# Optimization experiments

Hardware: AMD Instinct MI355X
Metric: run time of the kernel (lower is better)

## Reference

```python
import jax, jax.numpy as jnp
import numpy as np

NB_RADIUSES = 24
SIGMA = 0.1


def setup_inputs() -> dict:
    key = jax.random.key(0)
    k1, k2, k3 = jax.random.split(key, 3)
    nb, nf, nx, ny, nz = 2, 2, 256, 256, 16
    x = jax.random.uniform(k1, (nb, nf, nx, ny, nz), dtype=jnp.float32)
    # center of mass: real part is the column coordinate (in [0, ny)),
    # imag part is the row coordinate (in [0, nx)) -- keep centers inside the plane
    com_real = jax.random.uniform(k2, (nb, nf, nz), dtype=jnp.float32) * ny
    com_imag = jax.random.uniform(k3, (nb, nf, nz), dtype=jnp.float32) * nx
    return {"x": x, "com_real": com_real, "com_imag": com_imag}


def reference(x, com_real, com_imag):
    nb, nf, nx, ny, nz = x.shape
    # complex plan: real = index % ny (column), imag = index // ny (row)
    col = jnp.arange(ny, dtype=jnp.float32)   # real axis
    row = jnp.arange(nx, dtype=jnp.float32)   # imag axis
    # centered plan, broadcast to (nb, nf, nx, ny, nz)
    dx = col[None, None, None, :, None] - com_real[:, :, None, None, :]
    dy = row[None, None, :, None, None] - com_imag[:, :, None, None, :]
    theta = jnp.arctan2(dy, dx)           # arg(centered_plan)
    theta_neg = jnp.arctan2(-dy, -dx)     # arg(-centered_plan)

    # angles i*(2pi/nr) - pi; branch selection identical to the torch code
    angles = np.arange(NB_RADIUSES) * (2.0 * np.pi / NB_RADIUSES) - np.pi
    use_neg = (angles > 0.5 * np.pi) | (angles < -0.5 * np.pi)
    targets = np.where(angles > 0.5 * np.pi, angles - np.pi,
                       np.where(angles < -0.5 * np.pi, angles + np.pi, angles))
    use_neg = jnp.asarray(use_neg)
    targets = jnp.asarray(targets.astype(np.float32))

    # select angle field per radius: (R, nb, nf, nx, ny, nz)
    sel = jnp.where(use_neg[:, None, None, None, None, None],
                    theta_neg[None], theta[None])
    coef = jnp.float32(1.0 / (SIGMA * np.sqrt(2.0 * np.pi)))
    diff = sel - targets[:, None, None, None, None, None]
    w = coef * jnp.exp(-(diff ** 2) / jnp.float32(2.0 * SIGMA ** 2))

    # gaussian-weighted reduction over the (x, y) plane, keep z
    s = jnp.einsum('Rbfxyz,bfxyz->bfRz', w, x)
    return jnp.sqrt(2.0 * s)
```

## Files before the change

kernel.cpp:

```cpp
#include <hip/hip_runtime.h>
#include <math.h>

#define NR 24
#define NBATCH 2
#define NFEAT 2
#define NX 256
#define NY 256
#define NZ 16

constexpr double DPI = 3.141592653589793;

struct Tgts { float t[NR]; int neg[NR]; };

constexpr Tgts make_tgts() {
    Tgts r{};
    for (int i = 0; i < NR; ++i) {
        double a = (double)i * (2.0 * DPI / 24.0) - DPI;
        int neg = (a > 0.5 * DPI) || (a < -0.5 * DPI);
        double t = a;
        if (a > 0.5 * DPI)       t = a - DPI;
        else if (a < -0.5 * DPI) t = a + DPI;
        r.t[i]   = (float)t;
        r.neg[i] = neg;
    }
    return r;
}
constexpr Tgts TG = make_tgts();

__global__ __launch_bounds__(256) void grx_partial(
    const float* __restrict__ x,
    const float* __restrict__ com_real,
    const float* __restrict__ com_imag,
    float* __restrict__ ws)
{
    const int tid = threadIdx.x;
    const int z   = tid & 15;
    const int c0  = tid >> 4;
    const int row = blockIdx.x & (NX - 1);
    const int bf  = blockIdx.x >> 8;

    const float comr = com_real[bf * NZ + z];
    const float comi = com_imag[bf * NZ + z];
    const float dy   = (float)row - comi;

    const float KE  = -50.0f;
    const float PIF = 3.14159265358979323846f;

    float acc[NR];
    #pragma unroll
    for (int r = 0; r < NR; ++r) acc[r] = 0.0f;

    const float* xp = x + ((size_t)(bf * NX + row)) * (NY * NZ);

    #pragma unroll 4
    for (int k = 0; k < 16; ++k) {
        const int col  = c0 + (k << 4);
        const float xv = xp[col * NZ + z];
        const float dx = (float)col - comr;
        const float th  = atan2f(dy, dx);
        const float thn = th - copysignf(PIF, th);
        #pragma unroll
        for (int r = 0; r < NR; ++r) {
            const float sel = TG.neg[r] ? thn : th;
            const float d   = sel - TG.t[r];
            acc[r] += __expf(d * d * KE) * xv;
        }
    }

    __shared__ float red[256 * NR];
    #pragma unroll
    for (int r = 0; r < NR; ++r) red[tid * NR + r] = acc[r];
    __syncthreads();

    for (int o = tid; o < NR * NZ; o += 256) {
        const int r  = o >> 4;
        const int zz = o & 15;
        float s = 0.0f;
        #pragma unroll
        for (int c = 0; c < 16; ++c)
            s += red[(c * 16 + zz) * NR + r];
        atomicAdd(&ws[(bf * NR + r) * NZ + zz], s);
    }
}

__global__ void grx_finalize(const float* __restrict__ ws, float* __restrict__ out, int n)
{
    const int i = blockIdx.x * blockDim.x + threadIdx.x;
    if (i < n) {
        const float coef = 3.9894228040143270f;
        out[i] = sqrtf(2.0f * coef * ws[i]);
    }
}

extern "C" void kernel_launch(void* const* d_in, const int* in_sizes, int n_in,
                              void* d_out, int out_size, void* d_ws, size_t ws_size,
                              hipStream_t stream)
{
    const float* x  = (const float*)d_in[0];
    const float* cr = (const float*)d_in[1];
    const float* ci = (const float*)d_in[2];
    float* out = (float*)d_out;
    float* ws  = (float*)d_ws;

    const int nout = NBATCH * NFEAT * NR * NZ;
    hipMemsetAsync(ws, 0, nout * sizeof(float), stream);

    grx_partial<<<dim3(NBATCH * NFEAT * NX), dim3(256), 0, stream>>>(x, cr, ci, ws);
    grx_finalize<<<dim3((nout + 255) / 256), dim3(256), 0, stream>>>(ws, out, nout);
}
```

Measured before the change: 91.79 us.

## Evaluate only three nearest angular bins with polynomial atan2 and split rows

Exploits the narrow Gaussian and periodic bin layout to compute only the nearest three target bins per element instead of all 24, accumulating into padded per-thread shared memory with dynamic indices. Replaces atan2f with a fast polynomial approximation and doubles the grid by splitting each row's columns across two blocks. Trades a tiny truncation/approximation error and shared-memory read-modify-writes for far fewer exp evaluations.

```diff
diff --git a/kernel.cpp b/kernel.cpp
--- a/kernel.cpp
+++ b/kernel.cpp
@@ -1,5 +1,4 @@
 #include <hip/hip_runtime.h>
-#include <math.h>
 
 #define NR 24
 #define NBATCH 2
@@ -7,25 +6,7 @@
 #define NX 256
 #define NY 256
 #define NZ 16
-
-constexpr double DPI = 3.141592653589793;
-
-struct Tgts { float t[NR]; int neg[NR]; };
-
-constexpr Tgts make_tgts() {
-    Tgts r{};
-    for (int i = 0; i < NR; ++i) {
-        double a = (double)i * (2.0 * DPI / 24.0) - DPI;
-        int neg = (a > 0.5 * DPI) || (a < -0.5 * DPI);
-        double t = a;
-        if (a > 0.5 * DPI)       t = a - DPI;
-        else if (a < -0.5 * DPI) t = a + DPI;
-        r.t[i]   = (float)t;
-        r.neg[i] = neg;
-    }
-    return r;
-}
-constexpr Tgts TG = make_tgts();
+#define PAD 25
 
 __global__ __launch_bounds__(256) void grx_partial(
     const float* __restrict__ x,
@@ -33,43 +14,71 @@
     const float* __restrict__ com_imag,
     float* __restrict__ ws)
 {
-    const int tid = threadIdx.x;
-    const int z   = tid & 15;
-    const int c0  = tid >> 4;
-    const int row = blockIdx.x & (NX - 1);
-    const int bf  = blockIdx.x >> 8;
+    __shared__ float red[256 * PAD];
+
+    const int tid  = threadIdx.x;
+    const int z    = tid & 15;
+    const int c0   = tid >> 4;
+    const int half = blockIdx.x & 1;
+    const int row  = (blockIdx.x >> 1) & (NX - 1);
+    const int bf   = blockIdx.x >> 9;
+
+    float* myred = &red[tid * PAD];
+    #pragma unroll
+    for (int i = 0; i < PAD; ++i) myred[i] = 0.0f;
 
     const float comr = com_real[bf * NZ + z];
     const float comi = com_imag[bf * NZ + z];
-    const float dy   = (float)row - comi;
+    const float dyv  = (float)row - comi;
+    const float ady  = fabsf(dyv);
 
-    const float KE  = -50.0f;
-    const float PIF = 3.14159265358979323846f;
-
-    float acc[NR];
-    #pragma unroll
-    for (int r = 0; r < NR; ++r) acc[r] = 0.0f;
+    const float PIF   = 3.14159265358979f;
+    const float PI_2  = 1.57079632679490f;
+    const float C_PSI = 3.81971863420549f;
+    const float C_E   = -3.4269908169872414f;
 
     const float* xp = x + ((size_t)(bf * NX + row)) * (NY * NZ);
 
-    #pragma unroll 4
-    for (int k = 0; k < 16; ++k) {
-        const int col  = c0 + (k << 4);
+    #pragma unroll 2
+    for (int kk = 0; kk < 8; ++kk) {
+        const int col  = c0 + ((half * 8 + kk) << 4);
         const float xv = xp[col * NZ + z];
-        const float dx = (float)col - comr;
-        const float th  = atan2f(dy, dx);
-        const float thn = th - copysignf(PIF, th);
-        #pragma unroll
-        for (int r = 0; r < NR; ++r) {
-            const float sel = TG.neg[r] ? thn : th;
-            const float d   = sel - TG.t[r];
-            acc[r] += __expf(d * d * KE) * xv;
-        }
+        const float dxv = (float)col - comr;
+
+        const float adx = fabsf(dxv);
+        const float mn  = fminf(adx, ady);
+        const float mx  = fmaxf(adx, ady);
+        const float t   = mn * __builtin_amdgcn_rcpf(fmaxf(mx, 1e-30f));
+        const float r2  = t * t;
+        float p = fmaf(r2, 0.0208351f, -0.0851330f);
+        p = fmaf(r2, p, 0.1801410f);
+        p = fmaf(r2, p, -0.3302995f);
+        p = fmaf(r2, p, 0.9998660f);
+        float th = t * p;
+        if (ady > adx)  th = PI_2 - th;
+        if (dxv < 0.0f) th = PIF - th;
+        th = copysignf(th, dyv);
+
+        const float psi = th * C_PSI;
+        const float nf  = rintf(psi);
+        const float f   = psi - nf;
+        const int base  = (int)nf + 12;
+
+        const float fm = f + 1.0f;
+        const float fp = f - 1.0f;
+        const float w0 = __expf(C_E * f  * f ) * xv;
+        const float wm = __expf(C_E * fm * fm) * xv;
+        const float wp = __expf(C_E * fp * fp) * xv;
+
+        int v0 = base - 1; v0 = (v0 < 0)   ? v0 + 24 : v0;
+        int v1 = base;     v1 = (v1 >= 24) ? v1 - 24 : v1;
+        int v2 = base + 1; v2 = (v2 >= 24) ? v2 - 24 : v2;
+
+        myred[v0] += wm;
+        myred[v1] += w0;
+        myred[v2] += wp;
     }
 
-    __shared__ float red[256 * NR];
-    #pragma unroll
-    for (int r = 0; r < NR; ++r) red[tid * NR + r] = acc[r];
     __syncthreads();
 
     for (int o = tid; o < NR * NZ; o += 256) {
@@ -78,7 +87,7 @@
         float s = 0.0f;
         #pragma unroll
         for (int c = 0; c < 16; ++c)
-            s += red[(c * 16 + zz) * NR + r];
+            s += red[(c * 16 + zz) * PAD + r];
         atomicAdd(&ws[(bf * NR + r) * NZ + zz], s);
     }
 }
@@ -103,8 +112,8 @@
     float* ws  = (float*)d_ws;
 
     const int nout = NBATCH * NFEAT * NR * NZ;
-    hipMemsetAsync(ws, 0, nout * sizeof(float), stream);
+    (void)hipMemsetAsync(ws, 0, nout * sizeof(float), stream);
 
-    grx_partial<<<dim3(NBATCH * NFEAT * NX), dim3(256), 0, stream>>>(x, cr, ci, ws);
+    grx_partial<<<dim3(NBATCH * NFEAT * NX * 2), dim3(256), 0, stream>>>(x, cr, ci, ws);
     grx_finalize<<<dim3((nout + 255) / 256), dim3(256), 0, stream>>>(ws, out, nout);
 }
```

Measured after the change: 90.06 us. About the same (-1.9%).
